# Optimization experiments

Hardware: AMD Instinct MI355X
Metric: run time of the kernel (lower is better)

The kernel has to match this reference:

```python
import jax, jax.numpy as jnp
import numpy as np

B, C, H, W = 4, 256, 128, 128
SP, HEADS = 4, 2
SCALE = (C // HEADS) ** -0.5  # module uses full dim//num_heads, not per-branch head dim
EPS = 1e-4
CB = C // 2  # channels per strip branch


def setup_inputs() -> dict:
    key = jax.random.key(0)
    ks = jax.random.split(key, 8)
    return {
        "x": jax.random.normal(ks[0], (B, C, H, W), jnp.float32),
        "ln_g": jnp.ones((C,), jnp.float32),
        "ln_b": jnp.zeros((C,), jnp.float32),
        "w_qkv": jax.random.normal(ks[1], (C, 3 * C), jnp.float32) * 0.02,
        "lepe_w1": jax.random.normal(ks[2], (CB, 1, 3, 3), jnp.float32) * 0.1,
        "lepe_b1": jnp.zeros((CB,), jnp.float32),
        "lepe_w2": jax.random.normal(ks[3], (CB, 1, 3, 3), jnp.float32) * 0.1,
        "lepe_b2": jnp.zeros((CB,), jnp.float32),
        "proj_w": jax.random.normal(ks[4], (C, C), jnp.float32) * 0.02,
        "proj_b": jnp.zeros((C,), jnp.float32),
    }


def _strip_branch(q, k, v, h, hsp, w, wsp, lepe_w, lepe_b):
    # q,k,v: [B, L=h*hsp*w*wsp, CB]; channel layout is (c head) -> head fastest
    cd = CB // HEADS
    nwin = B * h * w

    def to_win(t):  # -> [(b h w), head, hsp*wsp, cd]
        t = t.reshape(B, h, hsp, w, wsp, cd, HEADS)
        t = t.transpose(0, 1, 3, 6, 2, 4, 5)  # B,h,w,head,hsp,wsp,cd
        return t.reshape(nwin, HEADS, hsp * wsp, cd)

    qw, kw, vw = to_win(q), to_win(k), to_win(v)

    # LePE: depthwise 3x3 conv on v laid out as [(b h w), (c head), hsp, wsp]
    vim = vw.reshape(nwin, HEADS, hsp, wsp, cd).transpose(0, 4, 1, 2, 3)
    vim = vim.reshape(nwin, CB, hsp, wsp)
    lepe = jax.lax.conv_general_dilated(vim, lepe_w, (1, 1), 'SAME',
                                        feature_group_count=CB)
    lepe = lepe + lepe_b[None, :, None, None]
    lepe = lepe.reshape(nwin, cd, HEADS, hsp, wsp).transpose(0, 2, 3, 4, 1)
    lepe = lepe.reshape(nwin, HEADS, hsp * wsp, cd)

    attn = jax.nn.softmax(jnp.einsum('whqc,whkc->whqk', qw * SCALE, kw), axis=-1)
    o = jnp.einsum('whqk,whkc->whqc', attn, vw) + lepe
    # back to b (c head) (h hsp) (w wsp)
    o = o.reshape(B, h, w, HEADS, hsp, wsp, cd)
    o = o.transpose(0, 6, 3, 1, 4, 2, 5).reshape(B, CB, h * hsp, w * wsp)
    return o


def reference(x, ln_g, ln_b, w_qkv, lepe_w1, lepe_b1, lepe_w2, lepe_b2, proj_w, proj_b):
    # tokens [B, H*W, C]
    xp = x.transpose(0, 2, 3, 1).reshape(B, H * W, C)
    mu = xp.mean(-1, keepdims=True)
    var = ((xp - mu) ** 2).mean(-1, keepdims=True)
    xp = (xp - mu) * jax.lax.rsqrt(var + EPS) * ln_g + ln_b

    qkv = xp @ w_qkv
    q, k, v = jnp.split(qkv, 3, axis=-1)

    # branch 1: horizontal strips (h=1, hsp=H, w=W/SP, wsp=SP) on first channel half
    x1 = _strip_branch(q[..., :CB], k[..., :CB], v[..., :CB],
                       1, H, W // SP, SP, lepe_w1, lepe_b1)
    # branch 2: vertical strips (h=H/SP, hsp=SP, w=1, wsp=W) on second half
    x2 = _strip_branch(q[..., CB:], k[..., CB:], v[..., CB:],
                       H // SP, SP, 1, W, lepe_w2, lepe_b2)

    xc = jnp.concatenate([x1, x2], axis=1)  # [B, C, H, W]
    out = jnp.einsum('bchw,oc->bohw', xc, proj_w) + proj_b[None, :, None, None]
    return out
```

## Files before the change

kernel.cpp:

```cpp
#include <hip/hip_runtime.h>
#include <stdint.h>

#define T_ 65536
#define HW_ 16384
#define SCALE_F 0.08838834764831845f
#define EPS_ 1e-4f

typedef unsigned short u16;
typedef unsigned int u32;
typedef __attribute__((ext_vector_type(4))) float f32x4;
typedef __attribute__((ext_vector_type(8))) __bf16 bf16x8v;

union frag_u { u16 h[8]; bf16x8v v; uint4 q4; };

__device__ __forceinline__ float bf2f(u16 h) {
    union { u32 u; float f; } x; x.u = ((u32)h) << 16; return x.f;
}
__device__ __forceinline__ u16 f2bf(float f) {
    union { u32 u; float f; } x; x.f = f;
    u32 u = x.u;
    return (u16)((u + 0x7FFFu + ((u >> 16) & 1u)) >> 16);
}
__device__ __forceinline__ f32x4 mfma_b(bf16x8v a, bf16x8v b, f32x4 c) {
    return __builtin_amdgcn_mfma_f32_16x16x32_bf16(a, b, c, 0, 0, 0);
}

__device__ __forceinline__ int u2t(int u, int br) {
    if (br == 1) return u;
    int b = u >> 14, rr = u & 16383;
    int s = rr >> 9, rem = rr & 511;
    int y = rem >> 2, xl = rem & 3;
    return (b << 14) + (y << 7) + (s << 2) + xl;
}
__device__ __forceinline__ int t2u0(int t) {
    int b = t >> 14, rr = t & 16383;
    int y = rr >> 7, x = rr & 127;
    return (b << 14) + ((x >> 2) << 9) + (y << 2) + (x & 3);
}

__global__ void sentinel_kernel(float* out, float code) {
    if (blockIdx.x == 0 && threadIdx.x == 0) out[0] = code;
}

__global__ __launch_bounds__(256) void wconv_kernel(const float* __restrict__ w,
        const float* __restrict__ pw, u16* __restrict__ wt, u16* __restrict__ pwc) {
    __shared__ float lds[64 * 65];
    int bid = blockIdx.x;
    int tid = threadIdx.x;
    if (bid < 48) {
        int c0 = (bid % 12) * 64, k0 = (bid / 12) * 64;
        for (int i = 0; i < 16; ++i) {
            int e = i * 256 + tid;
            int k = e >> 6, c = e & 63;
            lds[k * 65 + c] = w[(size_t)(k0 + k) * 768 + c0 + c];
        }
        __syncthreads();
        for (int i = 0; i < 16; ++i) {
            int e = i * 256 + tid;
            int c = e >> 6, k = e & 63;
            wt[(size_t)(c0 + c) * 256 + k0 + k] = f2bf(lds[k * 65 + c]);
        }
    } else {
        int base = (bid - 48) * 2048;
        for (int i = 0; i < 8; ++i) {
            int e = base + i * 256 + tid;
            int m = e >> 8, ks = e & 255;
            int c = (ks < 128) ? (2 * (ks & 63) + (ks >> 6))
                               : (128 + 2 * ((ks - 128) & 63) + ((ks - 128) >> 6));
            pwc[e] = f2bf(pw[(size_t)m * 256 + c]);
        }
    }
}

__global__ __launch_bounds__(512, 2) void ln_kernel(const float* __restrict__ x,
        const float* __restrict__ g, const float* __restrict__ bta, u16* __restrict__ xn) {
    __shared__ float reds[8][260];
    __shared__ float redss[8][260];
    __shared__ float mus[256];
    __shared__ float rstds[256];
    int tid = threadIdx.x, lane = tid & 63, w = tid >> 6;
    int w32 = w * 32;
    int tok0 = blockIdx.x * 256 + lane * 4;
    int b = tok0 >> 14, hw = tok0 & 16383;
    const float* xb = x + (size_t)b * 256 * HW_ + hw;
    float4 v[32];
    #pragma unroll
    for (int j = 0; j < 32; ++j)
        v[j] = *(const float4*)(xb + (size_t)(w32 + j) * HW_);
    float s0 = 0.f, s1 = 0.f, s2 = 0.f, s3 = 0.f;
    float q0 = 0.f, q1 = 0.f, q2 = 0.f, q3 = 0.f;
    #pragma unroll
    for (int j = 0; j < 32; ++j) {
        s0 += v[j].x; q0 += v[j].x * v[j].x;
        s1 += v[j].y; q1 += v[j].y * v[j].y;
        s2 += v[j].z; q2 += v[j].z * v[j].z;
        s3 += v[j].w; q3 += v[j].w * v[j].w;
    }
    *(float4*)&reds[w][lane * 4]  = make_float4(s0, s1, s2, s3);
    *(float4*)&redss[w][lane * 4] = make_float4(q0, q1, q2, q3);
    __syncthreads();
    if (tid < 256) {
        float S = 0.f, SS = 0.f;
        #pragma unroll
        for (int p = 0; p < 8; ++p) { S += reds[p][tid]; SS += redss[p][tid]; }
        float mu = S * (1.f / 256.f);
        float var = SS * (1.f / 256.f) - mu * mu;
        mus[tid] = mu;
        rstds[tid] = rsqrtf(var + EPS_);
    }
    __syncthreads();
    float4 mu4 = *(const float4*)&mus[lane * 4];
    float4 rs4 = *(const float4*)&rstds[lane * 4];
    float mk[4] = {mu4.x, mu4.y, mu4.z, mu4.w};
    float rk[4] = {rs4.x, rs4.y, rs4.z, rs4.w};
    #pragma unroll
    for (int k = 0; k < 4; ++k) {
        u16 tmp[32] __attribute__((aligned(16)));
        #pragma unroll
        for (int j = 0; j < 32; ++j) {
            int c = w32 + j;
            float xv = (k == 0) ? v[j].x : (k == 1) ? v[j].y : (k == 2) ? v[j].z : v[j].w;
            tmp[j] = f2bf((xv - mk[k]) * rk[k] * g[c] + bta[c]);
        }
        u16* o = xn + (size_t)(tok0 + k) * 256 + w32;
        *(uint4*)(o)      = *(const uint4*)&tmp[0];
        *(uint4*)(o + 8)  = *(const uint4*)&tmp[8];
        *(uint4*)(o + 16) = *(const uint4*)&tmp[16];
        *(uint4*)(o + 24) = *(const uint4*)&tmp[24];
    }
}

__global__ __launch_bounds__(256) void qkv_gemm(const u16* __restrict__ wt,
        const u16* __restrict__ xn, u16* __restrict__ qkt, u16* __restrict__ vpl, int br) {
    __shared__ __align__(16) u16 a_tile[4 * 129 * 8];
    __shared__ __align__(16) u16 b_tile[4 * 129 * 8];
    int my = blockIdx.y;
    int n0 = blockIdx.x * 128;
    int tid = threadIdx.x;
    int lane = tid & 63, wid = tid >> 6;
    int wm = wid >> 1, wn = wid & 1;
    int l15 = lane & 15, quad = lane >> 4;
    int colbase = (my == 0) ? (br * 128) : (my == 1 ? (256 + br * 128) : (512 + br * 128));
    f32x4 acc[4][4] = {};
    for (int k0 = 0; k0 < 256; k0 += 32) {
        __syncthreads();
        for (int ch = tid; ch < 512; ch += 256) {
            int gg = ch >> 7, row = ch & 127;
            *(uint4*)&a_tile[(gg * 129 + row) * 8] =
                *(const uint4*)&wt[(size_t)(colbase + row) * 256 + k0 + gg * 8];
        }
        for (int ch = tid; ch < 512; ch += 256) {
            int row = ch >> 2, gg = ch & 3;
            int t = u2t(n0 + row, br);
            *(uint4*)&b_tile[(gg * 129 + row) * 8] =
                *(const uint4*)&xn[(size_t)t * 256 + k0 + gg * 8];
        }
        __syncthreads();
        bf16x8v af[4], bf[4];
        #pragma unroll
        for (int i = 0; i < 4; ++i) {
            af[i] = *(const bf16x8v*)&a_tile[(quad * 129 + wm * 64 + i * 16 + l15) * 8];
            bf[i] = *(const bf16x8v*)&b_tile[(quad * 129 + wn * 64 + i * 16 + l15) * 8];
        }
        #pragma unroll
        for (int i = 0; i < 4; ++i)
            #pragma unroll
            for (int j = 0; j < 4; ++j)
                acc[i][j] = mfma_b(af[i], bf[j], acc[i][j]);
    }
    if (my < 2) {
        int cb2 = my * 128;
        #pragma unroll
        for (int i = 0; i < 4; ++i) {
            #pragma unroll
            for (int r = 0; r < 4; ++r) {
                int cl = wm * 64 + i * 16 + quad * 4 + r;
                int col = cb2 + ((cl & 1) << 6) + (cl >> 1);
                #pragma unroll
                for (int j = 0; j < 4; ++j) {
                    int u = n0 + wn * 64 + j * 16 + l15;
                    qkt[(size_t)u * 256 + col] = f2bf(acc[i][j][r]);
                }
            }
        }
    } else {
        #pragma unroll
        for (int i = 0; i < 4; ++i) {
            int pbase = wm * 64 + i * 16 + quad * 4;
            #pragma unroll
            for (int j = 0; j < 4; ++j) {
                int u = n0 + wn * 64 + j * 16 + l15;
                #pragma unroll
                for (int r = 0; r < 4; ++r)
                    vpl[(size_t)(pbase + r) * T_ + u] = f2bf(acc[i][j][r]);
            }
        }
    }
}

__global__ __launch_bounds__(512, 4) void attn_kernel(const u16* __restrict__ qkt,
        const u16* __restrict__ vpl, u16* __restrict__ xcb, int stride) {
    __shared__ __align__(16) u16 k_area[2][128 * 72];
    __shared__ __align__(16) u16 v_lds[2][64 * 136];
    int bid = blockIdx.x;
    int id2 = (bid & 7) * 128 + (bid >> 3);
    int window = id2 >> 3, h = (id2 >> 2) & 1, qq = id2 & 3;
    int wbase = window * 512;
    int tid = threadIdx.x, lane = tid & 63, wid = tid >> 6;
    int l15 = lane & 15, quad = lane >> 4;

    frag_u af[2];
    {
        size_t qrow = (size_t)(wbase + qq * 128 + wid * 16 + l15) * 256 + h * 64 + quad * 8;
        af[0].q4 = *(const uint4*)&qkt[qrow];
        af[1].q4 = *(const uint4*)&qkt[qrow + 32];
    }
    for (int idx = tid; idx < 1024; idx += 512) {
        int tok = idx >> 3, c8 = (idx & 7) * 8;
        *(uint4*)&k_area[0][tok * 72 + c8] =
            *(const uint4*)&qkt[(size_t)(wbase + tok) * 256 + 128 + h * 64 + c8];
    }
    for (int idx = tid; idx < 1024; idx += 512) {
        int cd = idx >> 4, k8 = (idx & 15) * 8;
        *(uint4*)&v_lds[0][cd * 136 + k8] =
            *(const uint4*)&vpl[(size_t)(2 * cd + h) * T_ + wbase + k8];
    }
    __syncthreads();

    float m[4] = {-1e30f, -1e30f, -1e30f, -1e30f};
    float l[4] = {0.f, 0.f, 0.f, 0.f};
    f32x4 acc_o[4] = {};
    for (int ch = 0; ch < 4; ++ch) {
        int cur = ch & 1, nxt = cur ^ 1;
        if (ch < 3) {
            for (int idx = tid; idx < 1024; idx += 512) {
                int tok = idx >> 3, c8 = (idx & 7) * 8;
                *(uint4*)&k_area[nxt][tok * 72 + c8] =
                    *(const uint4*)&qkt[(size_t)(wbase + (ch + 1) * 128 + tok) * 256 + 128 + h * 64 + c8];
            }
            for (int idx = tid; idx < 1024; idx += 512) {
                int cd = idx >> 4, k8 = (idx & 15) * 8;
                *(uint4*)&v_lds[nxt][cd * 136 + k8] =
                    *(const uint4*)&vpl[(size_t)(2 * cd + h) * T_ + wbase + (ch + 1) * 128 + k8];
            }
        }
        f32x4 s[8];
        #pragma unroll
        for (int kt = 0; kt < 8; ++kt) {
            f32x4 z = {0.f, 0.f, 0.f, 0.f};
            bf16x8v b0 = *(const bf16x8v*)&k_area[cur][(kt * 16 + l15) * 72 + quad * 8];
            bf16x8v b1 = *(const bf16x8v*)&k_area[cur][(kt * 16 + l15) * 72 + 32 + quad * 8];
            z = mfma_b(af[0].v, b0, z);
            z = mfma_b(af[1].v, b1, z);
            s[kt] = z;
        }
        float cmx[4] = {-1e30f, -1e30f, -1e30f, -1e30f};
        #pragma unroll
        for (int kt = 0; kt < 8; ++kt)
            #pragma unroll
            for (int r = 0; r < 4; ++r) cmx[r] = fmaxf(cmx[r], s[kt][r]);
        #pragma unroll
        for (int d = 1; d < 16; d <<= 1)
            #pragma unroll
            for (int r = 0; r < 4; ++r) cmx[r] = fmaxf(cmx[r], __shfl_xor(cmx[r], d, 16));
        float alpha[4];
        #pragma unroll
        for (int r = 0; r < 4; ++r) {
            float mn = fmaxf(m[r], cmx[r]);
            alpha[r] = __expf((m[r] - mn) * SCALE_F);
            m[r] = mn;
        }
        float ps[4] = {0.f, 0.f, 0.f, 0.f};
        #pragma unroll
        for (int kt = 0; kt < 8; ++kt)
            #pragma unroll
            for (int r = 0; r < 4; ++r) {
                float p = __expf((s[kt][r] - m[r]) * SCALE_F);
                s[kt][r] = p;
                ps[r] += p;
            }
        #pragma unroll
        for (int r = 0; r < 4; ++r) l[r] = l[r] * alpha[r] + ps[r];
        #pragma unroll
        for (int cs = 0; cs < 4; ++cs)
            #pragma unroll
            for (int r = 0; r < 4; ++r) acc_o[cs][r] *= alpha[r];
        __syncthreads();
        u16* p_lds = &k_area[cur][wid * 1152];
        #pragma unroll
        for (int half = 0; half < 2; ++half) {
            #pragma unroll
            for (int kt4 = 0; kt4 < 4; ++kt4)
                #pragma unroll
                for (int rr = 0; rr < 4; ++rr)
                    p_lds[(quad * 4 + rr) * 72 + kt4 * 16 + l15] = f2bf(s[half * 4 + kt4][rr]);
            #pragma unroll
            for (int k32 = 0; k32 < 2; ++k32) {
                bf16x8v pa = *(const bf16x8v*)&p_lds[l15 * 72 + k32 * 32 + quad * 8];
                #pragma unroll
                for (int cs = 0; cs < 4; ++cs) {
                    bf16x8v vf = *(const bf16x8v*)&v_lds[cur]
                        [(cs * 16 + l15) * 136 + half * 64 + k32 * 32 + quad * 8];
                    acc_o[cs] = mfma_b(pa, vf, acc_o[cs]);
                }
            }
        }
        __syncthreads();
    }
    float linv[4];
    #pragma unroll
    for (int r = 0; r < 4; ++r) {
        float v = l[r];
        #pragma unroll
        for (int d = 1; d < 16; d <<= 1) v += __shfl_xor(v, d, 16);
        linv[r] = 1.f / v;
    }
    #pragma unroll
    for (int cs = 0; cs < 4; ++cs) {
        int col = h * 64 + cs * 16 + l15;
        #pragma unroll
        for (int r = 0; r < 4; ++r) {
            int u = wbase + qq * 128 + wid * 16 + quad * 4 + r;
            xcb[(size_t)u * stride + col] = f2bf(acc_o[cs][r] * linv[r]);
        }
    }
}

__global__ __launch_bounds__(512) void lepe_kernel(const u16* __restrict__ vpl,
        const float* __restrict__ lw, const float* __restrict__ lb,
        u16* __restrict__ xcb, int stride, int br) {
    __shared__ __align__(16) u16 o_s[512 * 72];
    int hh = blockIdx.x & 1, wdw = blockIdx.x >> 1;
    int wbase = wdw * 512;
    int tid = threadIdx.x;
    int xd = (br == 0) ? 4 : 128;
    for (int i = 0; i < 8; ++i) {
        int g = i * 512 + tid;
        int cd = g >> 6, u0 = (g & 63) * 8;
        int cl = 2 * cd + hh;
        const u16* vp = vpl + (size_t)cl * T_ + wbase;
        const float* wp = lw + cl * 9;
        float bias = lb[cl];
        float acc[8];
        #pragma unroll
        for (int j = 0; j < 8; ++j) acc[j] = bias;
        #pragma unroll
        for (int r = -1; r <= 1; ++r) {
            int offA = u0 + r * xd;
            int offB = offA + 4;
            float m[8];
            if (offA >= 0 && offA <= 508) {
                uint2 va = *(const uint2*)&vp[offA];
                u16 ha[4]; *(uint2*)ha = va;
                #pragma unroll
                for (int j = 0; j < 4; ++j) m[j] = bf2f(ha[j]);
            } else { m[0] = m[1] = m[2] = m[3] = 0.f; }
            if (offB >= 0 && offB <= 508) {
                uint2 vb = *(const uint2*)&vp[offB];
                u16 hb[4]; *(uint2*)hb = vb;
                #pragma unroll
                for (int j = 0; j < 4; ++j) m[4 + j] = bf2f(hb[j]);
            } else { m[4] = m[5] = m[6] = m[7] = 0.f; }
            float le = 0.f, re = 0.f;
            if (br == 1) {
                if (offA >= 0 && offA <= 508 && (u0 & 127) != 0)   le = bf2f(vp[offA - 1]);
                if (offB >= 0 && offB <= 508 && (u0 & 127) != 120) re = bf2f(vp[offB + 4]);
            }
            float w0 = wp[(r + 1) * 3 + 0], w1 = wp[(r + 1) * 3 + 1], w2 = wp[(r + 1) * 3 + 2];
            #pragma unroll
            for (int j = 0; j < 8; ++j) {
                float lv, rv2;
                if (j == 0) lv = (br == 0) ? 0.f : le;
                else        lv = (br == 0 && (j & 3) == 0) ? 0.f : m[j - 1];
                if (j == 7) rv2 = (br == 0) ? 0.f : re;
                else        rv2 = (br == 0 && (j & 3) == 3) ? 0.f : m[j + 1];
                acc[j] += w0 * lv + w1 * m[j] + w2 * rv2;
            }
        }
        int cdp = cd ^ (((u0 >> 3) & 7) << 3);
        #pragma unroll
        for (int j = 0; j < 8; ++j)
            o_s[(u0 + j) * 72 + cdp] = f2bf(acc[j]);
    }
    __syncthreads();
    for (int i = 0; i < 8; ++i) {
        int c = i * 512 + tid;
        int tok = c >> 3, cg = c & 7;
        int cgp = cg ^ ((tok >> 3) & 7);
        uint4 lv = *(const uint4*)&o_s[tok * 72 + cgp * 8];
        u16 lh[8]; *(uint4*)lh = lv;
        u16* p = &xcb[(size_t)(wbase + tok) * stride + hh * 64 + cg * 8];
        uint4 gv = *(const uint4*)p;
        u16 gh[8]; *(uint4*)gh = gv;
        u16 oh[8] __attribute__((aligned(16)));
        #pragma unroll
        for (int j = 0; j < 8; ++j) oh[j] = f2bf(bf2f(gh[j]) + bf2f(lh[j]));
        *(uint4*)p = *(const uint4*)oh;
    }
}

__global__ __launch_bounds__(256) void proj_kernel(const u16* __restrict__ pwc,
        const u16* __restrict__ xc0, const u16* __restrict__ xnov,
        const float* __restrict__ pb, float* __restrict__ out) {
    __shared__ __align__(16) u16 a_tile[4 * 129 * 8];
    __shared__ __align__(16) u16 b_tile[4 * 129 * 8];
    int m0 = blockIdx.y * 128, n0 = blockIdx.x * 128;
    int tid = threadIdx.x;
    int lane = tid & 63, wid = tid >> 6;
    int wm = wid >> 1, wn = wid & 1;
    int l15 = lane & 15, quad = lane >> 4;
    f32x4 acc[4][4] = {};
    for (int k0 = 0; k0 < 256; k0 += 32) {
        __syncthreads();
        for (int ch = tid; ch < 512; ch += 256) {
            int gg = ch >> 7, row = ch & 127;
            *(uint4*)&a_tile[(gg * 129 + row) * 8] =
                *(const uint4*)&pwc[(size_t)(m0 + row) * 256 + k0 + gg * 8];
        }
        for (int ch = tid; ch < 512; ch += 256) {
            int row = ch >> 2, gg = ch & 3;
            int t = n0 + row;
            uint4 v;
            if (k0 < 128) v = *(const uint4*)&xc0[(size_t)t2u0(t) * 128 + k0 + gg * 8];
            else          v = *(const uint4*)&xnov[(size_t)t * 256 + k0 + gg * 8];
            *(uint4*)&b_tile[(gg * 129 + row) * 8] = v;
        }
        __syncthreads();
        bf16x8v af[4], bf[4];
        #pragma unroll
        for (int i = 0; i < 4; ++i) {
            af[i] = *(const bf16x8v*)&a_tile[(quad * 129 + wm * 64 + i * 16 + l15) * 8];
            bf[i] = *(const bf16x8v*)&b_tile[(quad * 129 + wn * 64 + i * 16 + l15) * 8];
        }
        #pragma unroll
        for (int i = 0; i < 4; ++i)
            #pragma unroll
            for (int j = 0; j < 4; ++j)
                acc[i][j] = mfma_b(af[i], bf[j], acc[i][j]);
    }
    #pragma unroll
    for (int i = 0; i < 4; ++i) {
        int mbase = m0 + wm * 64 + i * 16 + quad * 4;
        #pragma unroll
        for (int j = 0; j < 4; ++j) {
            int nc = n0 + wn * 64 + j * 16 + l15;
            #pragma unroll
            for (int r = 0; r < 4; ++r) {
                int m = mbase + r;
                out[((size_t)(nc >> 14) * 256 + m) * HW_ + (nc & 16383)] = acc[i][j][r] + pb[m];
            }
        }
    }
}

extern "C" void kernel_launch(void* const* d_in, const int* in_sizes, int n_in,
                              void* d_out, int out_size, void* d_ws, size_t ws_size,
                              hipStream_t stream) {
    const float* x     = (const float*)d_in[0];
    const float* ln_g  = (const float*)d_in[1];
    const float* ln_b  = (const float*)d_in[2];
    const float* w_qkv = (const float*)d_in[3];
    const float* lw1   = (const float*)d_in[4];
    const float* lb1   = (const float*)d_in[5];
    const float* lw2   = (const float*)d_in[6];
    const float* lb2   = (const float*)d_in[7];
    const float* pw    = (const float*)d_in[8];
    const float* pb    = (const float*)d_in[9];
    float* out = (float*)d_out;
    u16* out_u16 = (u16*)d_out;
    char* ws = (char*)d_ws;

    if (ws_size < 67108864) {
        sentinel_kernel<<<dim3(1), dim3(64), 0, stream>>>(out, 1.0e6f + (float)(ws_size >> 20));
        return;
    }

    u16* xn  = (u16*)ws;
    u16* xc0 = (u16*)(ws + 33554432);
    u16* wt  = (u16*)(ws + 50331648);
    u16* pwc = wt + 196608;
    u16* vpl = out_u16;
    u16* qkt = out_u16 + 8388608;

    wconv_kernel<<<dim3(80), dim3(256), 0, stream>>>(w_qkv, pw, wt, pwc);
    ln_kernel<<<dim3(256), dim3(512), 0, stream>>>(x, ln_g, ln_b, xn);
    qkv_gemm<<<dim3(512, 3), dim3(256), 0, stream>>>(wt, xn, qkt, vpl, 0);
    attn_kernel<<<dim3(1024), dim3(512), 0, stream>>>(qkt, vpl, xc0, 128);
    lepe_kernel<<<dim3(256), dim3(512), 0, stream>>>(vpl, lw1, lb1, xc0, 128, 0);
    qkv_gemm<<<dim3(512, 3), dim3(256), 0, stream>>>(wt, xn, qkt, vpl, 1);
    attn_kernel<<<dim3(1024), dim3(512), 0, stream>>>(qkt, vpl, xn + 128, 256);
    lepe_kernel<<<dim3(256), dim3(512), 0, stream>>>(vpl, lw2, lb2, xn + 128, 256, 1);
    proj_kernel<<<dim3(512, 2), dim3(256), 0, stream>>>(pwc, xc0, xn, pb, out);
}
```

Before: 425.4 us.

## Double-buffer GEMM tiles with direct global-to-LDS loads in qkv and proj

The qkv and projection GEMMs now stage their A and B tiles with global_load_lds straight into shared memory, skipping the register round trip. Each GEMM keeps two LDS buffers, so the next K-slice is fetched while MFMAs run on the current one, and one barrier per iteration is dropped. The new LDS layout is unpadded with a 64-byte row stride, which may add bank conflicts on the fragment reads. Correctness relies on the barrier waiting for the outstanding direct-to-LDS loads.

```diff
diff --git a/kernel.cpp b/kernel.cpp
--- a/kernel.cpp
+++ b/kernel.cpp
@@ -23,6 +23,11 @@
 }
 __device__ __forceinline__ f32x4 mfma_b(bf16x8v a, bf16x8v b, f32x4 c) {
     return __builtin_amdgcn_mfma_f32_16x16x32_bf16(a, b, c, 0, 0, 0);
+}
+__device__ __forceinline__ void gl_lds16(const u16* g, u16* l) {
+    __builtin_amdgcn_global_load_lds(
+        (const __attribute__((address_space(1))) void*)g,
+        (__attribute__((address_space(3))) void*)l, 16, 0, 0);
 }
 
 __device__ __forceinline__ int u2t(int u, int br) {
@@ -132,8 +137,8 @@
 
 __global__ __launch_bounds__(256) void qkv_gemm(const u16* __restrict__ wt,
         const u16* __restrict__ xn, u16* __restrict__ qkt, u16* __restrict__ vpl, int br) {
-    __shared__ __align__(16) u16 a_tile[4 * 129 * 8];
-    __shared__ __align__(16) u16 b_tile[4 * 129 * 8];
+    __shared__ __align__(16) u16 a_tile[2][128 * 32];
+    __shared__ __align__(16) u16 b_tile[2][128 * 32];
     int my = blockIdx.y;
     int n0 = blockIdx.x * 128;
     int tid = threadIdx.x;
@@ -141,26 +146,33 @@
     int wm = wid >> 1, wn = wid & 1;
     int l15 = lane & 15, quad = lane >> 4;
     int colbase = (my == 0) ? (br * 128) : (my == 1 ? (256 + br * 128) : (512 + br * 128));
+    int srow = tid >> 2, sgg = tid & 3;
+    const u16* gA0 = wt + (size_t)(colbase + srow) * 256 + sgg * 8;
+    const u16* gA1 = gA0 + (size_t)64 * 256;
+    const u16* gB0 = xn + (size_t)u2t(n0 + srow, br) * 256 + sgg * 8;
+    const u16* gB1 = xn + (size_t)u2t(n0 + srow + 64, br) * 256 + sgg * 8;
+    int lb0 = wid * 1024, lb1 = 4096 + wid * 1024;
+    gl_lds16(gA0, (u16*)((char*)&a_tile[0][0] + lb0));
+    gl_lds16(gA1, (u16*)((char*)&a_tile[0][0] + lb1));
+    gl_lds16(gB0, (u16*)((char*)&b_tile[0][0] + lb0));
+    gl_lds16(gB1, (u16*)((char*)&b_tile[0][0] + lb1));
     f32x4 acc[4][4] = {};
-    for (int k0 = 0; k0 < 256; k0 += 32) {
+    for (int ks = 0; ks < 8; ++ks) {
         __syncthreads();
-        for (int ch = tid; ch < 512; ch += 256) {
-            int gg = ch >> 7, row = ch & 127;
-            *(uint4*)&a_tile[(gg * 129 + row) * 8] =
-                *(const uint4*)&wt[(size_t)(colbase + row) * 256 + k0 + gg * 8];
-        }
-        for (int ch = tid; ch < 512; ch += 256) {
-            int row = ch >> 2, gg = ch & 3;
-            int t = u2t(n0 + row, br);
-            *(uint4*)&b_tile[(gg * 129 + row) * 8] =
-                *(const uint4*)&xn[(size_t)t * 256 + k0 + gg * 8];
-        }
-        __syncthreads();
+        int cur = ks & 1;
+        if (ks < 7) {
+            int k0 = (ks + 1) * 32;
+            int nb = cur ^ 1;
+            gl_lds16(gA0 + k0, (u16*)((char*)&a_tile[nb][0] + lb0));
+            gl_lds16(gA1 + k0, (u16*)((char*)&a_tile[nb][0] + lb1));
+            gl_lds16(gB0 + k0, (u16*)((char*)&b_tile[nb][0] + lb0));
+            gl_lds16(gB1 + k0, (u16*)((char*)&b_tile[nb][0] + lb1));
+        }
         bf16x8v af[4], bf[4];
         #pragma unroll
         for (int i = 0; i < 4; ++i) {
-            af[i] = *(const bf16x8v*)&a_tile[(quad * 129 + wm * 64 + i * 16 + l15) * 8];
-            bf[i] = *(const bf16x8v*)&b_tile[(quad * 129 + wn * 64 + i * 16 + l15) * 8];
+            af[i] = *(const bf16x8v*)&a_tile[cur][(wm * 64 + i * 16 + l15) * 32 + quad * 8];
+            bf[i] = *(const bf16x8v*)&b_tile[cur][(wn * 64 + i * 16 + l15) * 32 + quad * 8];
         }
         #pragma unroll
         for (int i = 0; i < 4; ++i)
@@ -402,35 +414,44 @@
 __global__ __launch_bounds__(256) void proj_kernel(const u16* __restrict__ pwc,
         const u16* __restrict__ xc0, const u16* __restrict__ xnov,
         const float* __restrict__ pb, float* __restrict__ out) {
-    __shared__ __align__(16) u16 a_tile[4 * 129 * 8];
-    __shared__ __align__(16) u16 b_tile[4 * 129 * 8];
+    __shared__ __align__(16) u16 a_tile[2][128 * 32];
+    __shared__ __align__(16) u16 b_tile[2][128 * 32];
     int m0 = blockIdx.y * 128, n0 = blockIdx.x * 128;
     int tid = threadIdx.x;
     int lane = tid & 63, wid = tid >> 6;
     int wm = wid >> 1, wn = wid & 1;
     int l15 = lane & 15, quad = lane >> 4;
+    int srow = tid >> 2, sgg = tid & 3;
+    const u16* gA0 = pwc + (size_t)(m0 + srow) * 256 + sgg * 8;
+    const u16* gA1 = gA0 + (size_t)64 * 256;
+    const u16* gB0lo = xc0 + (size_t)t2u0(n0 + srow) * 128 + sgg * 8;
+    const u16* gB1lo = xc0 + (size_t)t2u0(n0 + srow + 64) * 128 + sgg * 8;
+    const u16* gB0hi = xnov + (size_t)(n0 + srow) * 256 + sgg * 8;
+    const u16* gB1hi = xnov + (size_t)(n0 + srow + 64) * 256 + sgg * 8;
+    int lb0 = wid * 1024, lb1 = 4096 + wid * 1024;
+    gl_lds16(gA0, (u16*)((char*)&a_tile[0][0] + lb0));
+    gl_lds16(gA1, (u16*)((char*)&a_tile[0][0] + lb1));
+    gl_lds16(gB0lo, (u16*)((char*)&b_tile[0][0] + lb0));
+    gl_lds16(gB1lo, (u16*)((char*)&b_tile[0][0] + lb1));
     f32x4 acc[4][4] = {};
-    for (int k0 = 0; k0 < 256; k0 += 32) {
+    for (int ks = 0; ks < 8; ++ks) {
         __syncthreads();
-        for (int ch = tid; ch < 512; ch += 256) {
-            int gg = ch >> 7, row = ch & 127;
-            *(uint4*)&a_tile[(gg * 129 + row) * 8] =
-                *(const uint4*)&pwc[(size_t)(m0 + row) * 256 + k0 + gg * 8];
-        }
-        for (int ch = tid; ch < 512; ch += 256) {
-            int row = ch >> 2, gg = ch & 3;
-            int t = n0 + row;
-            uint4 v;
-            if (k0 < 128) v = *(const uint4*)&xc0[(size_t)t2u0(t) * 128 + k0 + gg * 8];
-            else          v = *(const uint4*)&xnov[(size_t)t * 256 + k0 + gg * 8];
-            *(uint4*)&b_tile[(gg * 129 + row) * 8] = v;
-        }
-        __syncthreads();
+        int cur = ks & 1;
+        if (ks < 7) {
+            int k0 = (ks + 1) * 32;
+            int nb = cur ^ 1;
+            gl_lds16(gA0 + k0, (u16*)((char*)&a_tile[nb][0] + lb0));
+            gl_lds16(gA1 + k0, (u16*)((char*)&a_tile[nb][0] + lb1));
+            const u16* b0 = (k0 < 128) ? (gB0lo + k0) : (gB0hi + k0);
+            const u16* b1 = (k0 < 128) ? (gB1lo + k0) : (gB1hi + k0);
+            gl_lds16(b0, (u16*)((char*)&b_tile[nb][0] + lb0));
+            gl_lds16(b1, (u16*)((char*)&b_tile[nb][0] + lb1));
+        }
         bf16x8v af[4], bf[4];
         #pragma unroll
         for (int i = 0; i < 4; ++i) {
-            af[i] = *(const bf16x8v*)&a_tile[(quad * 129 + wm * 64 + i * 16 + l15) * 8];
-            bf[i] = *(const bf16x8v*)&b_tile[(quad * 129 + wn * 64 + i * 16 + l15) * 8];
+            af[i] = *(const bf16x8v*)&a_tile[cur][(wm * 64 + i * 16 + l15) * 32 + quad * 8];
+            bf[i] = *(const bf16x8v*)&b_tile[cur][(wn * 64 + i * 16 + l15) * 32 + quad * 8];
         }
         #pragma unroll
         for (int i = 0; i < 4; ++i)
```

Result: faster. 415.4 us (-2.3%).
